# Optimization experiments

Measured on AMD Instinct MI355X. Metric: run time of the kernel, lower is better.

Reference implementation:

```python
import jax, jax.numpy as jnp
import numpy as np

MODES = 128
WIDTH = 128
L_SEG = 20
M_CHEB = 8


def _cft_mag(x):
    # x: [B, C, N] real. Faithful port of vectorized_batched_cft_decomposed
    # (L=20 segments, M=8 Chebyshev nodes), restricted to the first MODES
    # frequencies (the only ones consumed downstream). Returns mean-|CFT|
    # over channels: [B, MODES]. Output is detached in the original code.
    n = x.shape[-1]
    t = jnp.linspace(0.0, 1.0, n)
    freqs = jnp.arange(MODES, dtype=jnp.float32)  # rfftfreq(n, d=1/n)[:MODES]
    seg_len = 1.0 / L_SEG
    a = jnp.linspace(0.0, 1.0, L_SEG + 1)[:-1]  # [L] segment starts
    k = jnp.arange(M_CHEB, dtype=jnp.float32)
    nodes = -jnp.cos((2.0 * k + 1.0) * jnp.pi / (2.0 * M_CHEB))  # [M]
    T = jnp.cos(k[:, None] * jnp.arccos(nodes)[None, :])  # [M(k), M(node)]
    w_prime = freqs * (2.0 * jnp.pi * seg_len / 2.0)  # [F]
    exp_q = jnp.exp(-1j * nodes[:, None] * w_prime[None, :])  # [M, F]
    cheb_w = (T @ exp_q) * (seg_len / 2.0)  # [M, F] complex
    shift = jnp.exp(-1j * 2.0 * jnp.pi * freqs[None, :] * a[:, None])  # [L, F]
    W = shift[:, None, :] * cheb_w[None, :, :]  # [L, M, F]
    # quadrature sample points and linear interpolation from the grid t
    t_seg = a[:, None] + seg_len / 2.0 * (nodes[None, :] + 1.0)  # [L, M]
    right = jnp.minimum(jnp.searchsorted(t, t_seg.reshape(-1)), n - 1).reshape(L_SEG, M_CHEB)
    left = jnp.maximum(right - 1, 0)
    tl, tr = t[left], t[right]
    denom = jnp.where(tr - tl == 0.0, 1.0, tr - tl)
    w_r = (t_seg - tl) / denom
    w_l = 1.0 - w_r
    sig = w_l[None, None] * x[:, :, left] + w_r[None, None] * x[:, :, right]  # [B,C,L,M]
    spec = jnp.einsum('bclm,lmf->bcf', sig.astype(jnp.complex64), W)  # [B,C,F]
    spec = jax.lax.stop_gradient(spec)  # .detach() in the original
    return jnp.mean(jnp.abs(spec), axis=1)  # [B, MODES]


def _forward(x, fc0_W, fc0_b, gate_W, gate_b, wA_re, wA_im, wB_re, wB_im,
             conv_W, conv_b, fc1_W, fc1_b, fc2_W, fc2_b):
    B, N, _ = x.shape
    grid = jnp.broadcast_to(jnp.linspace(0.0, 1.0, N)[None, :, None], (B, N, 1))
    h = jnp.concatenate([x, grid], axis=-1) @ fc0_W.T + fc0_b  # [B,N,W]
    h = h.transpose(0, 2, 1)  # [B,W,N]
    n_f = N // 2 + 1
    for i in range(4):
        mag = _cft_mag(h)  # [B, MODES], detached
        gate = jax.nn.sigmoid(mag @ gate_W[i].T + gate_b[i])  # [B, W]
        # weights1 = gate*A + (1-gate)*B, then the original einsum
        # 'bix,bioy->box' sums weights over the mode axis y; fold that sum
        # into the (in,out) matrices first.
        wA = (wA_re[i] + 1j * wA_im[i]).sum(-1)  # [in, out]
        wB = (wB_re[i] + 1j * wB_im[i]).sum(-1)
        Wg = gate[:, None, :] * wA[None] + (1.0 - gate[:, None, :]) * wB[None]  # [B,in,out]
        h_ft = jnp.fft.rfft(h)  # [B,W,n_f]
        out_modes = jnp.einsum('bif,bio->bof', h_ft[:, :, :MODES], Wg)
        out_ft = jnp.zeros((B, WIDTH, n_f), jnp.complex64).at[:, :, :MODES].set(out_modes)
        x1 = jnp.fft.irfft(out_ft, n=N)  # [B,W,N]
        x2 = jnp.einsum('bcn,oc->bon', h, conv_W[i]) + conv_b[i][None, :, None]
        h = x1 + x2
        if i < 3:
            h = jax.nn.gelu(h, approximate=False)
    h = h.transpose(0, 2, 1)  # [B,N,W]
    h = jax.nn.gelu(h @ fc1_W.T + fc1_b, approximate=False)
    return h @ fc2_W.T + fc2_b  # [B,N,1]


def setup_inputs() -> dict:
    key = jax.random.key(0)
    ks = jax.random.split(key, 16)
    B, N = 64, 4096
    scale = 1.0 / (WIDTH * WIDTH)
    d = {}
    d['x'] = jax.random.normal(ks[0], (B, N, 1), jnp.float32)
    d['fc0_W'] = jax.random.normal(ks[1], (WIDTH, 2), jnp.float32) * 0.1
    d['fc0_b'] = jnp.zeros((WIDTH,), jnp.float32)
    d['gate_W'] = jax.random.normal(ks[2], (4, WIDTH, MODES), jnp.float32) * 0.05
    d['gate_b'] = jnp.zeros((4, WIDTH), jnp.float32)
    d['wA_re'] = jax.random.uniform(ks[3], (4, WIDTH, WIDTH, MODES), jnp.float32) * scale
    d['wA_im'] = jax.random.uniform(ks[4], (4, WIDTH, WIDTH, MODES), jnp.float32) * scale
    d['wB_re'] = jax.random.uniform(ks[5], (4, WIDTH, WIDTH, MODES), jnp.float32) * scale
    d['wB_im'] = jax.random.uniform(ks[6], (4, WIDTH, WIDTH, MODES), jnp.float32) * scale
    d['conv_W'] = jax.random.normal(ks[7], (4, WIDTH, WIDTH), jnp.float32) * 0.05
    d['conv_b'] = jnp.zeros((4, WIDTH), jnp.float32)
    d['fc1_W'] = jax.random.normal(ks[8], (128, WIDTH), jnp.float32) * 0.05
    d['fc1_b'] = jnp.zeros((128,), jnp.float32)
    d['fc2_W'] = jax.random.normal(ks[9], (1, 128), jnp.float32) * 0.05
    d['fc2_b'] = jnp.zeros((1,), jnp.float32)
    return d


def reference(x, fc0_W, fc0_b, gate_W, gate_b, wA_re, wA_im, wB_re, wB_im,
              conv_W, conv_b, fc1_W, fc1_b, fc2_W, fc2_b):
    return _forward(x, fc0_W, fc0_b, gate_W, gate_b, wA_re, wA_im, wB_re, wB_im,
                    conv_W, conv_b, fc1_W, fc1_b, fc2_W, fc2_b)
```

## Files before the change

### kernel.cpp

```cpp
#include <hip/hip_runtime.h>
#include <math.h>

#define B_SZ 64
#define WID 128
#define NPT 4096
#define MODES 128
#define LSEG 20
#define MCH 8
#define LM 160

typedef _Float16 half8 __attribute__((ext_vector_type(8)));
typedef float f32x4 __attribute__((ext_vector_type(4)));

#define LO_SCALE 2048.0f
#define LO_INV   (1.0f/2048.0f)

static constexpr size_t BY_F    = 0;
static constexpr size_t BY_wsum = BY_F + 8388608;
static constexpr size_t BY_Wcre = BY_wsum + 1048576;
static constexpr size_t BY_Wcim = BY_Wcre + 81920;
static constexpr size_t BY_wl   = BY_Wcim + 81920;
static constexpr size_t BY_wr   = BY_wl + 1024;
static constexpr size_t BY_li   = BY_wr + 1024;
static constexpr size_t BY_magp = BY_li + 1024;
static constexpr size_t BY_gate = BY_magp + 524288;
static constexpr size_t BY_hh   = BY_gate + 32768;
static constexpr size_t BY_hl   = BY_hh + 67108864;
static constexpr size_t BY_Tfh  = BY_hl + 67108864;
static constexpr size_t BY_Tfl  = BY_Tfh + 2097152;
static constexpr size_t BY_Tih  = BY_Tfl + 2097152;
static constexpr size_t BY_Til  = BY_Tih + 2097152;
static constexpr size_t BY_Xh   = BY_Til + 2097152;
static constexpr size_t BY_Xl   = BY_Xh + 4194304;
static constexpr size_t BY_cWh  = BY_Xl + 4194304;
static constexpr size_t BY_cWl  = BY_cWh + 131072;
static constexpr size_t BY_f1h  = BY_cWl + 131072;
static constexpr size_t BY_f1l  = BY_f1h + 32768;
static constexpr size_t BY_end  = BY_f1l + 32768;

__device__ __forceinline__ float gelu_f(float x){
    return 0.5f*x*(1.0f+erff(x*0.70710678118654752f));
}
__device__ __forceinline__ void split_f16(float v, _Float16& hi, _Float16& lo){
    hi = (_Float16)v;
    lo = (_Float16)((v - (float)hi)*LO_SCALE);
}

__global__ void k_tables(_Float16* __restrict__ Tfh, _Float16* __restrict__ Tfl,
                         _Float16* __restrict__ Tih, _Float16* __restrict__ Til){
    int idx = blockIdx.x*256 + threadIdx.x;
    int n = idx >> 8, k2 = idx & 255;
    int f = k2 >> 1;
    int m = (n*f) & 4095;
    double th = (double)m * (3.14159265358979323846/2048.0);
    double s, c; sincos(th, &s, &c);
    float vf = (k2&1) ? (float)(-s) : (float)c;
    _Float16 h1,l1; split_f16(vf, h1, l1);
    Tfh[(size_t)k2*4096 + n] = h1;
    Tfl[(size_t)k2*4096 + n] = l1;
    float vi;
    if (k2 == 0)      vi = 1.0f;
    else if (k2 == 1) vi = 0.0f;
    else              vi = vf;
    _Float16 h2,l2; split_f16(vi, h2, l2);
    Tih[(size_t)n*256 + k2] = h2;
    Til[(size_t)n*256 + k2] = l2;
}

__global__ void k_cft_tables(float* __restrict__ Wre, float* __restrict__ Wim,
                             float* __restrict__ wl, float* __restrict__ wr,
                             int* __restrict__ li){
    int idx = blockIdx.x*128 + threadIdx.x;
    if (idx >= LM*MODES) return;
    int lm = idx >> 7;  int f = idx & 127;
    int l = lm / MCH, m = lm % MCH;
    const double PI = 3.14159265358979323846;
    double nodes[8], Tm[8];
    #pragma unroll
    for (int j=0;j<8;j++){
        nodes[j] = -cos((2.0*j+1.0)*PI/16.0);
        Tm[j] = cos((double)m * acos(nodes[j]));
    }
    double wp = (double)f * PI * 0.05;
    double cwre=0.0, cwim=0.0;
    #pragma unroll
    for (int j=0;j<8;j++){
        double sj, cj; sincos(nodes[j]*wp, &sj, &cj);
        cwre += Tm[j]*cj;
        cwim -= Tm[j]*sj;
    }
    cwre *= 0.025; cwim *= 0.025;
    int r = (f*l) % 20;
    double sa = 2.0*PI*(double)r/20.0;
    double shre = cos(sa), shim = -sin(sa);
    Wre[lm*128+f] = (float)(shre*cwre - shim*cwim);
    Wim[lm*128+f] = (float)(shre*cwim + shim*cwre);
    if (f == 0){
        double v = (double)l/20.0 + 0.025*(nodes[m]+1.0);
        int rr = (int)ceil(v*4095.0);
        if (rr > 4095) rr = 4095;
        if (rr < 1) rr = 1;
        int le = rr-1;
        double tl = (double)le/4095.0, tr = (double)rr/4095.0;
        double wrv = (v - tl)/(tr - tl);
        li[lm] = le;
        wl[lm] = (float)(1.0 - wrv);
        wr[lm] = (float)wrv;
    }
}

__global__ void k_wsum(const float* __restrict__ wAre, const float* __restrict__ wAim,
                       const float* __restrict__ wBre, const float* __restrict__ wBim,
                       float* __restrict__ out){
    int row  = blockIdx.x*4 + (threadIdx.x>>6);
    int lane = threadIdx.x & 63;
    const float* src = (blockIdx.y==0)?wAre:(blockIdx.y==1)?wAim:(blockIdx.y==2)?wBre:wBim;
    float v = src[(size_t)row*128 + lane] + src[(size_t)row*128 + 64 + lane];
    #pragma unroll
    for (int o=32;o>0;o>>=1) v += __shfl_down(v, o);
    if (lane==0) out[(size_t)blockIdx.y*65536 + row] = v;
}

__global__ void k_wsplit(const float* __restrict__ convW, const float* __restrict__ fc1W,
                         _Float16* __restrict__ cWh, _Float16* __restrict__ cWl,
                         _Float16* __restrict__ f1h, _Float16* __restrict__ f1l){
    int idx = blockIdx.x*256 + threadIdx.x;
    if (idx < 65536){
        _Float16 hi,lo; split_f16(convW[idx], hi, lo);
        cWh[idx]=hi; cWl[idx]=lo;
    } else {
        int j = idx - 65536;
        _Float16 hi,lo; split_f16(fc1W[j], hi, lo);
        f1h[j]=hi; f1l[j]=lo;
    }
}

__global__ void k_h0(const float* __restrict__ x, const float* __restrict__ w0,
                     const float* __restrict__ b0,
                     _Float16* __restrict__ hh, _Float16* __restrict__ hl){
    int idx = blockIdx.x*256 + threadIdx.x;
    int n8 = idx & 511;
    int w  = (idx >> 9) & 127;
    int b  = idx >> 16;
    int n0 = n8*8;
    float w00 = w0[w*2], w01 = w0[w*2+1], bb = b0[w];
    const float* xr = &x[((size_t)b<<12) + n0];
    float4 x0 = *reinterpret_cast<const float4*>(xr);
    float4 x1 = *reinterpret_cast<const float4*>(xr+4);
    float xv[8]={x0.x,x0.y,x0.z,x0.w,x1.x,x1.y,x1.z,x1.w};
    half8 vh, vl;
    #pragma unroll
    for (int q=0;q<8;q++){
        float g = (float)(n0+q) * (1.0f/4095.0f);
        float v = xv[q]*w00 + g*w01 + bb;
        _Float16 hi,lo; split_f16(v,hi,lo);
        vh[q]=hi; vl[q]=lo;
    }
    size_t o = ((size_t)(b*128+w))*4096 + n0;
    *reinterpret_cast<half8*>(&hh[o]) = vh;
    *reinterpret_cast<half8*>(&hl[o]) = vl;
}

__global__ void k_cft(const _Float16* __restrict__ hh, const _Float16* __restrict__ hl,
                      const float* __restrict__ Wre, const float* __restrict__ Wim,
                      const float* __restrict__ wl, const float* __restrict__ wr,
                      const int* __restrict__ li, float* __restrict__ magp){
    int b = blockIdx.x, cg = blockIdx.y;
    int f = threadIdx.x;
    __shared__ float sig[LM];
    __shared__ float swl[LM], swr[LM];
    __shared__ int   sli[LM];
    for (int s=f; s<LM; s+=128){ swl[s]=wl[s]; swr[s]=wr[s]; sli[s]=li[s]; }
    __syncthreads();
    float acc = 0.f;
    for (int cc=0; cc<8; cc++){
        int c = cg*8 + cc;
        const _Float16* rh = hh + ((size_t)(b*128+c))*4096;
        const _Float16* rl = hl + ((size_t)(b*128+c))*4096;
        for (int s=f; s<LM; s+=128){
            int le = sli[s];
            float v0 = (float)rh[le]   + (float)rl[le]*LO_INV;
            float v1 = (float)rh[le+1] + (float)rl[le+1]*LO_INV;
            sig[s] = swl[s]*v0 + swr[s]*v1;
        }
        __syncthreads();
        float re=0.f, im=0.f;
        #pragma unroll 8
        for (int s=0;s<LM;s++){
            float sv = sig[s];
            re = fmaf(sv, Wre[s*128+f], re);
            im = fmaf(sv, Wim[s*128+f], im);
        }
        acc += sqrtf(re*re+im*im);
        __syncthreads();
    }
    magp[(b*16+cg)*128 + f] = acc;
}

__global__ void k_gate(const float* __restrict__ magp, const float* __restrict__ gW,
                       const float* __restrict__ gB, float* __restrict__ gate, int layer){
    int b = blockIdx.x, w = threadIdx.x;
    __shared__ float ms[128];
    float s = 0.f;
    #pragma unroll
    for (int g=0; g<16; g++) s += magp[(b*16+g)*128 + w];
    ms[w] = s * (1.0f/128.0f);
    __syncthreads();
    const float* gwr = gW + ((size_t)layer*128 + w)*128;
    float a = gB[layer*128 + w];
    #pragma unroll 8
    for (int fq=0; fq<128; fq++) a = fmaf(ms[fq], gwr[fq], a);
    gate[b*128+w] = 1.0f/(1.0f+expf(-a));
}

__global__ __launch_bounds__(256) void k_fdft(
        const _Float16* __restrict__ hh, const _Float16* __restrict__ hl,
        const _Float16* __restrict__ Tfh, const _Float16* __restrict__ Tfl,
        float* __restrict__ F){
    __shared__ _Float16 Ah[2][64][40], Al[2][64][40], Bh[2][64][40], Bl[2][64][40];
    int id = blockIdx.x;
    int swz = (id & 7)*64 + (id >> 3);
    int bx = swz & 3, by = swz >> 2;
    int col0 = bx*64, row0 = by*64;
    int tid = threadIdx.x;
    int lane = tid & 63, w = tid >> 6;
    int wr = (w>>1)*32, wc = (w&1)*32;
    int l15 = lane & 15, l4 = lane >> 4;
    f32x4 acc[2][2] = {}; f32x4 acc2[2][2] = {};
    int srow = tid >> 2, sseg = tid & 3;
    const _Float16* pa_h = hh  + (size_t)(row0+srow)*4096 + sseg*8;
    const _Float16* pa_l = hl  + (size_t)(row0+srow)*4096 + sseg*8;
    const _Float16* pb_h = Tfh + (size_t)(col0+srow)*4096 + sseg*8;
    const _Float16* pb_l = Tfl + (size_t)(col0+srow)*4096 + sseg*8;
    half8 Aah,Aal,Abh,Abl, Bah,Bal,Bbh,Bbl;
#define LOADK(sa,sal,sb,sbl,ck) do{ int kk=(ck)*32; \
    sa  = *reinterpret_cast<const half8*>(pa_h + kk); \
    sal = *reinterpret_cast<const half8*>(pa_l + kk); \
    sb  = *reinterpret_cast<const half8*>(pb_h + kk); \
    sbl = *reinterpret_cast<const half8*>(pb_l + kk); }while(0)
#define WRITEK(sa,sal,sb,sbl,buf) do{ \
    *reinterpret_cast<half8*>(&Ah[buf][srow][sseg*8]) = sa; \
    *reinterpret_cast<half8*>(&Al[buf][srow][sseg*8]) = sal; \
    *reinterpret_cast<half8*>(&Bh[buf][srow][sseg*8]) = sb; \
    *reinterpret_cast<half8*>(&Bl[buf][srow][sseg*8]) = sbl; }while(0)
#define MMF(buf) do{ \
    half8 fah[2], fal[2], fbh[2], fbl[2]; \
    _Pragma("unroll") for (int i=0;i<2;i++){ \
        fah[i] = *reinterpret_cast<const half8*>(&Ah[buf][wr + i*16 + l15][l4*8]); \
        fal[i] = *reinterpret_cast<const half8*>(&Al[buf][wr + i*16 + l15][l4*8]); \
        fbh[i] = *reinterpret_cast<const half8*>(&Bh[buf][wc + i*16 + l15][l4*8]); \
        fbl[i] = *reinterpret_cast<const half8*>(&Bl[buf][wc + i*16 + l15][l4*8]); } \
    _Pragma("unroll") for (int i=0;i<2;i++) \
        _Pragma("unroll") for (int j=0;j<2;j++){ \
            acc[i][j]  = __builtin_amdgcn_mfma_f32_16x16x32_f16(fah[i], fbh[j], acc[i][j], 0,0,0); \
            acc2[i][j] = __builtin_amdgcn_mfma_f32_16x16x32_f16(fah[i], fbl[j], acc2[i][j],0,0,0); \
            acc2[i][j] = __builtin_amdgcn_mfma_f32_16x16x32_f16(fal[i], fbh[j], acc2[i][j],0,0,0); } }while(0)
    LOADK(Aah,Aal,Abh,Abl, 0);
    WRITEK(Aah,Aal,Abh,Abl, 0);
    LOADK(Aah,Aal,Abh,Abl, 1);
    LOADK(Bah,Bal,Bbh,Bbl, 2);
    __syncthreads();
    for (int tt = 0; tt < 64; ++tt){
        int t = tt*2;
        MMF(0);
        WRITEK(Aah,Aal,Abh,Abl, 1);
        if (t+3 < 128) LOADK(Aah,Aal,Abh,Abl, t+3);
        __syncthreads();
        MMF(1);
        if (t+2 < 128) WRITEK(Bah,Bal,Bbh,Bbl, 0);
        if (t+4 < 128) LOADK(Bah,Bal,Bbh,Bbl, t+4);
        __syncthreads();
    }
#undef LOADK
#undef WRITEK
#undef MMF
    #pragma unroll
    for (int i=0;i<2;i++)
        #pragma unroll
        for (int j=0;j<2;j++)
            #pragma unroll
            for (int r=0;r<4;r++){
                int row = row0 + wr + i*16 + l4*4 + r;
                int col = col0 + wc + j*16 + l15;
                F[(size_t)row*256 + col] = acc[i][j][r] + acc2[i][j][r]*LO_INV;
            }
}

__global__ __launch_bounds__(256) void k_modemix(const float* __restrict__ F,
        const float* __restrict__ wsum, const float* __restrict__ gate,
        _Float16* __restrict__ Xh, _Float16* __restrict__ Xl, int layer){
    int b = blockIdx.x, og = blockIdx.y;
    __shared__ float Fs[16][256];
    __shared__ float Wa_re[128][8], Wa_im[128][8], Wb_re[128][8], Wb_im[128][8];
    int tid = threadIdx.x;
    for (int e=tid; e<1024; e+=256){
        int i = e>>3, oo = e&7;
        size_t base = ((size_t)layer*128 + i)*128 + og*8 + oo;
        Wa_re[i][oo] = wsum[0*65536 + base];
        Wa_im[i][oo] = wsum[1*65536 + base];
        Wb_re[i][oo] = wsum[2*65536 + base];
        Wb_im[i][oo] = wsum[3*65536 + base];
    }
    int f = tid & 127, half = tid >> 7;
    float pre[4]={},pim[4]={},qre[4]={},qim[4]={};
    for (int i0=0;i0<128;i0+=16){
        for (int e=tid; e<4096; e+=256){
            int ii = e >> 8, k2 = e & 255;
            Fs[ii][k2] = F[((size_t)(b*128 + i0+ii))*256 + k2];
        }
        __syncthreads();
        #pragma unroll
        for (int ii=0; ii<16; ii++){
            float fre = Fs[ii][2*f], fim = Fs[ii][2*f+1];
            int i = i0+ii;
            #pragma unroll
            for (int q=0;q<4;q++){
                int oo = half*4+q;
                float are=Wa_re[i][oo], aim=Wa_im[i][oo];
                float bre=Wb_re[i][oo], bim=Wb_im[i][oo];
                pre[q] = fmaf(fre, are, fmaf(-fim, aim, pre[q]));
                pim[q] = fmaf(fre, aim, fmaf( fim, are, pim[q]));
                qre[q] = fmaf(fre, bre, fmaf(-fim, bim, qre[q]));
                qim[q] = fmaf(fre, bim, fmaf( fim, bre, qim[q]));
            }
        }
        __syncthreads();
    }
    #pragma unroll
    for (int q=0;q<4;q++){
        int o = og*8 + half*4 + q;
        float g = gate[b*128+o];
        float xre = g*pre[q] + (1.f-g)*qre[q];
        float xim = g*pim[q] + (1.f-g)*qim[q];
        float s = (f==0) ? (1.0f/4096.0f) : (2.0f/4096.0f);
        xre *= s; xim *= s;
        if (f==0) xim = 0.f;
        size_t base = ((size_t)(b*128+o))*256 + 2*f;
        _Float16 h1,l1; split_f16(xre,h1,l1); Xh[base]=h1;   Xl[base]=l1;
        _Float16 h2,l2; split_f16(xim,h2,l2); Xh[base+1]=h2; Xl[base+1]=l2;
    }
}

__global__ __launch_bounds__(256) void k_flayer(
    const _Float16* __restrict__ Xh, const _Float16* __restrict__ Xl,
    const _Float16* __restrict__ Tih, const _Float16* __restrict__ Til,
    const _Float16* __restrict__ cWh, const _Float16* __restrict__ cWl,
    const float* __restrict__ convB,
    _Float16* __restrict__ hh, _Float16* __restrict__ hl,
    int layer, int applyGelu){
    __shared__ _Float16 As_h[2][128][40], As_l[2][128][40];
    __shared__ _Float16 Bs_h[2][64][40],  Bs_l[2][64][40];
    int n0 = blockIdx.x*64;
    int b  = blockIdx.y;
    int tid = threadIdx.x, lane = tid & 63, w = tid >> 6;
    int l15 = lane & 15, l4 = lane >> 4;
    int o0 = w*32;
    int aro = tid >> 2, asl = tid & 3;
    int ctc = tid >> 3, ctn = tid & 7;
    int ocp = ((tid >> 6) ^ (tid & 3));
    const _Float16* cA_h = cWh + (size_t)layer*16384 + (size_t)aro*128 + asl*8;
    const _Float16* cA_l = cWl + (size_t)layer*16384 + (size_t)aro*128 + asl*8;
    const _Float16* xA_h = Xh + ((size_t)(b*128 + aro))*256 + asl*8;
    const _Float16* xA_l = Xl + ((size_t)(b*128 + aro))*256 + asl*8;
    const _Float16* hB_h = hh + ((size_t)(b*128 + ctc))*4096 + n0 + ctn*8;
    const _Float16* hB_l = hl + ((size_t)(b*128 + ctc))*4096 + n0 + ctn*8;
    const _Float16* tB_h = Tih + (size_t)(n0 + aro)*256 + asl*8;
    const _Float16* tB_l = Til + (size_t)(n0 + aro)*256 + asl*8;
    f32x4 acc[2][4] = {}; f32x4 acc2[2][4] = {};
    half8 rA[6], rB[6];
#define LOADR(r,ck) do{ \
    if ((ck) < 4){ int kk = (ck)*32; \
        r[0] = *reinterpret_cast<const half8*>(cA_h + kk); \
        r[1] = *reinterpret_cast<const half8*>(cA_l + kk); \
        r[2] = *reinterpret_cast<const half8*>(cA_h + 64*128 + kk); \
        r[3] = *reinterpret_cast<const half8*>(cA_l + 64*128 + kk); \
        r[4] = *reinterpret_cast<const half8*>(hB_h + (size_t)(ck)*32*4096); \
        r[5] = *reinterpret_cast<const half8*>(hB_l + (size_t)(ck)*32*4096); \
    } else { int kk = ((ck)-4)*32; \
        r[0] = *reinterpret_cast<const half8*>(xA_h + kk); \
        r[1] = *reinterpret_cast<const half8*>(xA_l + kk); \
        r[2] = *reinterpret_cast<const half8*>(xA_h + 64*256 + kk); \
        r[3] = *reinterpret_cast<const half8*>(xA_l + 64*256 + kk); \
        r[4] = *reinterpret_cast<const half8*>(tB_h + kk); \
        r[5] = *reinterpret_cast<const half8*>(tB_l + kk); } }while(0)
#define WRITER(r,buf,ck) do{ \
    *reinterpret_cast<half8*>(&As_h[buf][aro][asl*8])    = r[0]; \
    *reinterpret_cast<half8*>(&As_l[buf][aro][asl*8])    = r[1]; \
    *reinterpret_cast<half8*>(&As_h[buf][aro+64][asl*8]) = r[2]; \
    *reinterpret_cast<half8*>(&As_l[buf][aro+64][asl*8]) = r[3]; \
    if ((ck) < 4){ \
        _Pragma("unroll") for (int j2=0;j2<8;j2++){ \
            int n = ctn*8 + j2; \
            Bs_h[buf][n][ocp*8 + (ctc&7)] = r[4][j2]; \
            Bs_l[buf][n][ocp*8 + (ctc&7)] = r[5][j2]; } \
    } else { \
        *reinterpret_cast<half8*>(&Bs_h[buf][aro][asl*8]) = r[4]; \
        *reinterpret_cast<half8*>(&Bs_l[buf][aro][asl*8]) = r[5]; } }while(0)
#define MML(buf,ck) do{ \
    half8 ah[2], al[2], bh[4], bl[4]; \
    _Pragma("unroll") for (int i=0;i<2;i++){ \
        ah[i] = *reinterpret_cast<const half8*>(&As_h[buf][o0+i*16+l15][l4*8]); \
        al[i] = *reinterpret_cast<const half8*>(&As_l[buf][o0+i*16+l15][l4*8]); } \
    if ((ck) < 4){ \
        _Pragma("unroll") for (int j=0;j<4;j++){ \
            int n = j*16 + l15; int sl = (l4 ^ ((n>>3)&3)); \
            bh[j] = *reinterpret_cast<const half8*>(&Bs_h[buf][n][sl*8]); \
            bl[j] = *reinterpret_cast<const half8*>(&Bs_l[buf][n][sl*8]); } \
    } else { \
        _Pragma("unroll") for (int j=0;j<4;j++){ \
            bh[j] = *reinterpret_cast<const half8*>(&Bs_h[buf][j*16+l15][l4*8]); \
            bl[j] = *reinterpret_cast<const half8*>(&Bs_l[buf][j*16+l15][l4*8]); } } \
    _Pragma("unroll") for (int i=0;i<2;i++) \
        _Pragma("unroll") for (int j=0;j<4;j++){ \
            acc[i][j]  = __builtin_amdgcn_mfma_f32_16x16x32_f16(ah[i], bh[j], acc[i][j], 0,0,0); \
            acc2[i][j] = __builtin_amdgcn_mfma_f32_16x16x32_f16(ah[i], bl[j], acc2[i][j],0,0,0); \
            acc2[i][j] = __builtin_amdgcn_mfma_f32_16x16x32_f16(al[i], bh[j], acc2[i][j],0,0,0); } }while(0)
    LOADR(rA, 0);
    WRITER(rA, 0, 0);
    LOADR(rA, 1);
    LOADR(rB, 2);
    __syncthreads();
    #pragma unroll
    for (int tt=0; tt<6; ++tt){
        const int t = 2*tt;
        MML(0, t);
        WRITER(rA, 1, t+1);
        if (t+3 < 12) LOADR(rA, t+3);
        __syncthreads();
        MML(1, t+1);
        if (t+2 < 12) WRITER(rB, 0, t+2);
        if (t+4 < 12) LOADR(rB, t+4);
        __syncthreads();
    }
#undef LOADR
#undef WRITER
#undef MML
    #pragma unroll
    for (int i=0;i<2;i++)
        #pragma unroll
        for (int j=0;j<4;j++)
            #pragma unroll
            for (int r=0;r<4;r++){
                int o = o0 + i*16 + l4*4 + r;
                int n = n0 + j*16 + l15;
                float v = acc[i][j][r] + acc2[i][j][r]*LO_INV + convB[layer*128+o];
                if (applyGelu) v = gelu_f(v);
                _Float16 hi,lo; split_f16(v,hi,lo);
                size_t oi = ((size_t)(b*128+o))*4096 + n;
                hh[oi] = hi; hl[oi] = lo;
            }
}

__global__ __launch_bounds__(256) void k_head(
        const _Float16* __restrict__ hh, const _Float16* __restrict__ hl,
        const _Float16* __restrict__ f1h, const _Float16* __restrict__ f1l,
        const float* __restrict__ fc1b,
        const float* __restrict__ fc2W, const float* __restrict__ fc2b,
        float* __restrict__ out){
    __shared__ _Float16 Bch[64][136], Bcl[64][136];
    __shared__ _Float16 Ash[128][40], Asl[128][40];
    __shared__ float red[16][64];
    int n0 = blockIdx.x*64;
    int b  = blockIdx.y;
    int tid = threadIdx.x, lane = tid & 63, w = tid >> 6;
    int l15 = lane & 15, l4 = lane >> 4;
    int j0 = w*32;
    {
        int c = tid & 127, nh = tid >> 7;
        const _Float16* rh = hh + ((size_t)(b*128+c))*4096 + n0 + nh*32;
        const _Float16* rl = hl + ((size_t)(b*128+c))*4096 + n0 + nh*32;
        #pragma unroll
        for (int j=0;j<4;j++){
            half8 vhv = *reinterpret_cast<const half8*>(rh + j*8);
            half8 vlv = *reinterpret_cast<const half8*>(rl + j*8);
            #pragma unroll
            for (int q=0;q<8;q++){
                int n = nh*32 + j*8 + q;
                Bch[n][c] = vhv[q];
                Bcl[n][c] = vlv[q];
            }
        }
    }
    __syncthreads();
    int so2 = tid >> 2, sseg = tid & 3;
    f32x4 acc[2][4] = {}; f32x4 acc2[2][4] = {};
    for (int k0=0;k0<128;k0+=32){
        #pragma unroll
        for (int p=0;p<2;p++){
            int o = p*64 + so2;
            *reinterpret_cast<half8*>(&Ash[o][sseg*8]) =
                *reinterpret_cast<const half8*>(&f1h[(size_t)o*128 + k0 + sseg*8]);
            *reinterpret_cast<half8*>(&Asl[o][sseg*8]) =
                *reinterpret_cast<const half8*>(&f1l[(size_t)o*128 + k0 + sseg*8]);
        }
        __syncthreads();
        half8 ah[2],al[2],bh[4],bl[4];
        #pragma unroll
        for (int i=0;i<2;i++){
            ah[i] = *reinterpret_cast<const half8*>(&Ash[j0+i*16+l15][l4*8]);
            al[i] = *reinterpret_cast<const half8*>(&Asl[j0+i*16+l15][l4*8]);
        }
        #pragma unroll
        for (int j=0;j<4;j++){
            bh[j] = *reinterpret_cast<const half8*>(&Bch[j*16+l15][k0+l4*8]);
            bl[j] = *reinterpret_cast<const half8*>(&Bcl[j*16+l15][k0+l4*8]);
        }
        #pragma unroll
        for (int i=0;i<2;i++)
            #pragma unroll
            for (int j=0;j<4;j++){
                acc[i][j]  = __builtin_amdgcn_mfma_f32_16x16x32_f16(ah[i], bh[j], acc[i][j], 0,0,0);
                acc2[i][j] = __builtin_amdgcn_mfma_f32_16x16x32_f16(ah[i], bl[j], acc2[i][j],0,0,0);
                acc2[i][j] = __builtin_amdgcn_mfma_f32_16x16x32_f16(al[i], bh[j], acc2[i][j],0,0,0);
            }
        __syncthreads();
    }
    float part[4];
    #pragma unroll
    for (int j=0;j<4;j++) part[j] = 0.f;
    #pragma unroll
    for (int i=0;i<2;i++){
        #pragma unroll
        for (int r=0;r<4;r++){
            int jj = j0 + i*16 + l4*4 + r;
            float b1 = fc1b[jj];
            float w2 = fc2W[jj];
            #pragma unroll
            for (int j=0;j<4;j++){
                float v = acc[i][j][r] + acc2[i][j][r]*LO_INV + b1;
                part[j] = fmaf(w2, gelu_f(v), part[j]);
            }
        }
    }
    #pragma unroll
    for (int j=0;j<4;j++) red[w*4+l4][j*16+l15] = part[j];
    __syncthreads();
    if (tid < 64){
        float s = fc2b[0];
        #pragma unroll
        for (int r=0;r<16;r++) s += red[r][tid];
        out[((size_t)b<<12) + n0 + tid] = s;
    }
}

extern "C" void kernel_launch(void* const* d_in, const int* in_sizes, int n_in,
                              void* d_out, int out_size, void* d_ws, size_t ws_size,
                              hipStream_t stream) {
    const float* x     = (const float*)d_in[0];
    const float* fc0W  = (const float*)d_in[1];
    const float* fc0b  = (const float*)d_in[2];
    const float* gateW = (const float*)d_in[3];
    const float* gateB = (const float*)d_in[4];
    const float* wAre  = (const float*)d_in[5];
    const float* wAim  = (const float*)d_in[6];
    const float* wBre  = (const float*)d_in[7];
    const float* wBim  = (const float*)d_in[8];
    const float* convW = (const float*)d_in[9];
    const float* convB = (const float*)d_in[10];
    const float* fc1W  = (const float*)d_in[11];
    const float* fc1b  = (const float*)d_in[12];
    const float* fc2W  = (const float*)d_in[13];
    const float* fc2b  = (const float*)d_in[14];
    float* out = (float*)d_out;
    char*  wsb = (char*)d_ws;

    float* F    = (float*)(wsb + BY_F);
    float* wsum = (float*)(wsb + BY_wsum);
    float* Wcre = (float*)(wsb + BY_Wcre);
    float* Wcim = (float*)(wsb + BY_Wcim);
    float* wl   = (float*)(wsb + BY_wl);
    float* wr   = (float*)(wsb + BY_wr);
    int*   li   = (int*)(wsb + BY_li);
    float* magp = (float*)(wsb + BY_magp);
    float* gate = (float*)(wsb + BY_gate);
    _Float16* hh  = (_Float16*)(wsb + BY_hh);
    _Float16* hl  = (_Float16*)(wsb + BY_hl);
    _Float16* Tfh = (_Float16*)(wsb + BY_Tfh);
    _Float16* Tfl = (_Float16*)(wsb + BY_Tfl);
    _Float16* Tih = (_Float16*)(wsb + BY_Tih);
    _Float16* Til = (_Float16*)(wsb + BY_Til);
    _Float16* Xh  = (_Float16*)(wsb + BY_Xh);
    _Float16* Xl  = (_Float16*)(wsb + BY_Xl);
    _Float16* cWh = (_Float16*)(wsb + BY_cWh);
    _Float16* cWl = (_Float16*)(wsb + BY_cWl);
    _Float16* f1h = (_Float16*)(wsb + BY_f1h);
    _Float16* f1l = (_Float16*)(wsb + BY_f1l);

    k_tables<<<4096, 256, 0, stream>>>(Tfh, Tfl, Tih, Til);
    k_cft_tables<<<160, 128, 0, stream>>>(Wcre, Wcim, wl, wr, li);
    k_wsum<<<dim3(16384,4), 256, 0, stream>>>(wAre, wAim, wBre, wBim, wsum);
    k_wsplit<<<320, 256, 0, stream>>>(convW, fc1W, cWh, cWl, f1h, f1l);
    k_h0<<<16384, 256, 0, stream>>>(x, fc0W, fc0b, hh, hl);

    for (int layer=0; layer<4; layer++){
        k_cft<<<dim3(64,16), 128, 0, stream>>>(hh, hl, Wcre, Wcim, wl, wr, li, magp);
        k_gate<<<64, 128, 0, stream>>>(magp, gateW, gateB, gate, layer);
        k_fdft<<<512, 256, 0, stream>>>(hh, hl, Tfh, Tfl, F);
        k_modemix<<<dim3(64,16), 256, 0, stream>>>(F, wsum, gate, Xh, Xl, layer);
        k_flayer<<<dim3(64,64), 256, 0, stream>>>(Xh, Xl, Tih, Til, cWh, cWl, convB,
                                                  hh, hl, layer, layer<3 ? 1:0);
    }
    k_head<<<dim3(64,64), 256, 0, stream>>>(hh, hl, f1h, f1l, fc1b, fc2W, fc2b, out);
    (void)in_sizes; (void)n_in; (void)out_size; (void)ws_size;
}
```

Before: 1.390 ms.

## Pre-swizzle DFT twiddle tables into MFMA fragment layout and load directly to registers

The forward and inverse DFT twiddle tables are now written in the per-lane MFMA B-fragment order, so k_fdft and k_flayer read B operands straight from global memory into registers instead of staging them through LDS. This removes the B-side LDS writes and reads and shrinks shared memory in k_fdft. The cost is more global or L2 traffic per wave, since each wave now fetches its own B fragments with no sharing across the block, and more registers for the prefetched fragments.

```diff
diff --git a/kernel.cpp b/kernel.cpp
--- a/kernel.cpp
+++ b/kernel.cpp
@@ -46,8 +46,8 @@
     lo = (_Float16)((v - (float)hi)*LO_SCALE);
 }
 
-__global__ void k_tables(_Float16* __restrict__ Tfh, _Float16* __restrict__ Tfl,
-                         _Float16* __restrict__ Tih, _Float16* __restrict__ Til){
+__global__ void k_tables(_Float16* __restrict__ Tffh, _Float16* __restrict__ Tffl,
+                         _Float16* __restrict__ Tifh, _Float16* __restrict__ Tifl){
     int idx = blockIdx.x*256 + threadIdx.x;
     int n = idx >> 8, k2 = idx & 255;
     int f = k2 >> 1;
@@ -55,16 +55,26 @@
     double th = (double)m * (3.14159265358979323846/2048.0);
     double s, c; sincos(th, &s, &c);
     float vf = (k2&1) ? (float)(-s) : (float)c;
-    _Float16 h1,l1; split_f16(vf, h1, l1);
-    Tfh[(size_t)k2*4096 + n] = h1;
-    Tfl[(size_t)k2*4096 + n] = l1;
+    {
+        _Float16 h1,l1; split_f16(vf, h1, l1);
+        int ct = k2>>4, ck = n>>5;
+        int lane = (((n>>3)&3)<<4) | (k2&15);
+        int j = n & 7;
+        size_t off = (((size_t)(ct*128 + ck))<<9) + lane*8 + j;
+        Tffh[off] = h1; Tffl[off] = l1;
+    }
     float vi;
     if (k2 == 0)      vi = 1.0f;
     else if (k2 == 1) vi = 0.0f;
     else              vi = vf;
-    _Float16 h2,l2; split_f16(vi, h2, l2);
-    Tih[(size_t)n*256 + k2] = h2;
-    Til[(size_t)n*256 + k2] = l2;
+    {
+        _Float16 h2,l2; split_f16(vi, h2, l2);
+        int nt = n>>4, ck2 = k2>>5;
+        int lane = (((k2>>3)&3)<<4) | (n&15);
+        int j = k2 & 7;
+        size_t off = (((size_t)(nt*8 + ck2))<<9) + lane*8 + j;
+        Tifh[off] = h2; Tifl[off] = l2;
+    }
 }
 
 __global__ void k_cft_tables(float* __restrict__ Wre, float* __restrict__ Wim,
@@ -215,64 +225,65 @@
 
 __global__ __launch_bounds__(256) void k_fdft(
         const _Float16* __restrict__ hh, const _Float16* __restrict__ hl,
-        const _Float16* __restrict__ Tfh, const _Float16* __restrict__ Tfl,
+        const _Float16* __restrict__ Tffh, const _Float16* __restrict__ Tffl,
         float* __restrict__ F){
-    __shared__ _Float16 Ah[2][64][40], Al[2][64][40], Bh[2][64][40], Bl[2][64][40];
+    __shared__ _Float16 Ah[2][64][40], Al[2][64][40];
     int id = blockIdx.x;
     int swz = (id & 7)*64 + (id >> 3);
     int bx = swz & 3, by = swz >> 2;
     int col0 = bx*64, row0 = by*64;
-    int tid = threadIdx.x;
-    int lane = tid & 63, w = tid >> 6;
+    int tid = threadIdx.x, lane = tid & 63, w = tid >> 6;
     int wr = (w>>1)*32, wc = (w&1)*32;
     int l15 = lane & 15, l4 = lane >> 4;
     f32x4 acc[2][2] = {}; f32x4 acc2[2][2] = {};
     int srow = tid >> 2, sseg = tid & 3;
-    const _Float16* pa_h = hh  + (size_t)(row0+srow)*4096 + sseg*8;
-    const _Float16* pa_l = hl  + (size_t)(row0+srow)*4096 + sseg*8;
-    const _Float16* pb_h = Tfh + (size_t)(col0+srow)*4096 + sseg*8;
-    const _Float16* pb_l = Tfl + (size_t)(col0+srow)*4096 + sseg*8;
-    half8 Aah,Aal,Abh,Abl, Bah,Bal,Bbh,Bbl;
-#define LOADK(sa,sal,sb,sbl,ck) do{ int kk=(ck)*32; \
-    sa  = *reinterpret_cast<const half8*>(pa_h + kk); \
-    sal = *reinterpret_cast<const half8*>(pa_l + kk); \
-    sb  = *reinterpret_cast<const half8*>(pb_h + kk); \
-    sbl = *reinterpret_cast<const half8*>(pb_l + kk); }while(0)
-#define WRITEK(sa,sal,sb,sbl,buf) do{ \
-    *reinterpret_cast<half8*>(&Ah[buf][srow][sseg*8]) = sa; \
-    *reinterpret_cast<half8*>(&Al[buf][srow][sseg*8]) = sal; \
-    *reinterpret_cast<half8*>(&Bh[buf][srow][sseg*8]) = sb; \
-    *reinterpret_cast<half8*>(&Bl[buf][srow][sseg*8]) = sbl; }while(0)
-#define MMF(buf) do{ \
-    half8 fah[2], fal[2], fbh[2], fbl[2]; \
+    const _Float16* pa_h = hh + (size_t)(row0+srow)*4096 + sseg*8;
+    const _Float16* pa_l = hl + (size_t)(row0+srow)*4096 + sseg*8;
+    int ct0 = (col0 + wc) >> 4;
+    const _Float16* pfh = Tffh + (size_t)lane*8;
+    const _Float16* pfl = Tffl + (size_t)lane*8;
+    half8 a0h,a0l,a1h,a1l;
+    half8 bf0[4], bf1[4];
+#define LOADA(xh,xl,ck) do{ \
+    xh = *reinterpret_cast<const half8*>(pa_h + (size_t)(ck)*32); \
+    xl = *reinterpret_cast<const half8*>(pa_l + (size_t)(ck)*32); }while(0)
+#define WRITEA(xh,xl,buf) do{ \
+    *reinterpret_cast<half8*>(&Ah[buf][srow][sseg*8]) = xh; \
+    *reinterpret_cast<half8*>(&Al[buf][srow][sseg*8]) = xl; }while(0)
+#define LOADB(dst,ck) do{ \
+    dst[0] = *reinterpret_cast<const half8*>(pfh + (((size_t)(ct0  )*128 + (ck))<<9)); \
+    dst[1] = *reinterpret_cast<const half8*>(pfh + (((size_t)(ct0+1)*128 + (ck))<<9)); \
+    dst[2] = *reinterpret_cast<const half8*>(pfl + (((size_t)(ct0  )*128 + (ck))<<9)); \
+    dst[3] = *reinterpret_cast<const half8*>(pfl + (((size_t)(ct0+1)*128 + (ck))<<9)); }while(0)
+#define MMF(buf,BF) do{ \
     _Pragma("unroll") for (int i=0;i<2;i++){ \
-        fah[i] = *reinterpret_cast<const half8*>(&Ah[buf][wr + i*16 + l15][l4*8]); \
-        fal[i] = *reinterpret_cast<const half8*>(&Al[buf][wr + i*16 + l15][l4*8]); \
-        fbh[i] = *reinterpret_cast<const half8*>(&Bh[buf][wc + i*16 + l15][l4*8]); \
-        fbl[i] = *reinterpret_cast<const half8*>(&Bl[buf][wc + i*16 + l15][l4*8]); } \
-    _Pragma("unroll") for (int i=0;i<2;i++) \
+        half8 fah = *reinterpret_cast<const half8*>(&Ah[buf][wr + i*16 + l15][l4*8]); \
+        half8 fal = *reinterpret_cast<const half8*>(&Al[buf][wr + i*16 + l15][l4*8]); \
         _Pragma("unroll") for (int j=0;j<2;j++){ \
-            acc[i][j]  = __builtin_amdgcn_mfma_f32_16x16x32_f16(fah[i], fbh[j], acc[i][j], 0,0,0); \
-            acc2[i][j] = __builtin_amdgcn_mfma_f32_16x16x32_f16(fah[i], fbl[j], acc2[i][j],0,0,0); \
-            acc2[i][j] = __builtin_amdgcn_mfma_f32_16x16x32_f16(fal[i], fbh[j], acc2[i][j],0,0,0); } }while(0)
-    LOADK(Aah,Aal,Abh,Abl, 0);
-    WRITEK(Aah,Aal,Abh,Abl, 0);
-    LOADK(Aah,Aal,Abh,Abl, 1);
-    LOADK(Bah,Bal,Bbh,Bbl, 2);
+            acc[i][j]  = __builtin_amdgcn_mfma_f32_16x16x32_f16(fah, BF[j],   acc[i][j], 0,0,0); \
+            acc2[i][j] = __builtin_amdgcn_mfma_f32_16x16x32_f16(fah, BF[2+j], acc2[i][j],0,0,0); \
+            acc2[i][j] = __builtin_amdgcn_mfma_f32_16x16x32_f16(fal, BF[j],   acc2[i][j],0,0,0); } } }while(0)
+    LOADA(a0h,a0l,0); WRITEA(a0h,a0l,0);
+    LOADA(a0h,a0l,1);
+    LOADA(a1h,a1l,2);
+    LOADB(bf0,0); LOADB(bf1,1);
     __syncthreads();
-    for (int tt = 0; tt < 64; ++tt){
+    for (int tt=0; tt<64; ++tt){
         int t = tt*2;
-        MMF(0);
-        WRITEK(Aah,Aal,Abh,Abl, 1);
-        if (t+3 < 128) LOADK(Aah,Aal,Abh,Abl, t+3);
-        __syncthreads();
-        MMF(1);
-        if (t+2 < 128) WRITEK(Bah,Bal,Bbh,Bbl, 0);
-        if (t+4 < 128) LOADK(Bah,Bal,Bbh,Bbl, t+4);
-        __syncthreads();
-    }
-#undef LOADK
-#undef WRITEK
+        MMF(0,bf0);
+        WRITEA(a0h,a0l,1);
+        if (t+2 < 128) LOADB(bf0, t+2);
+        if (t+3 < 128) LOADA(a0h,a0l, t+3);
+        __syncthreads();
+        MMF(1,bf1);
+        if (t+2 < 128) WRITEA(a1h,a1l,0);
+        if (t+3 < 128) LOADB(bf1, t+3);
+        if (t+4 < 128) LOADA(a1h,a1l, t+4);
+        __syncthreads();
+    }
+#undef LOADA
+#undef WRITEA
+#undef LOADB
 #undef MMF
     #pragma unroll
     for (int i=0;i<2;i++)
@@ -343,7 +354,7 @@
 
 __global__ __launch_bounds__(256) void k_flayer(
     const _Float16* __restrict__ Xh, const _Float16* __restrict__ Xl,
-    const _Float16* __restrict__ Tih, const _Float16* __restrict__ Til,
+    const _Float16* __restrict__ Tifh, const _Float16* __restrict__ Tifl,
     const _Float16* __restrict__ cWh, const _Float16* __restrict__ cWl,
     const float* __restrict__ convB,
     _Float16* __restrict__ hh, _Float16* __restrict__ hl,
@@ -364,25 +375,25 @@
     const _Float16* xA_l = Xl + ((size_t)(b*128 + aro))*256 + asl*8;
     const _Float16* hB_h = hh + ((size_t)(b*128 + ctc))*4096 + n0 + ctn*8;
     const _Float16* hB_l = hl + ((size_t)(b*128 + ctc))*4096 + n0 + ctn*8;
-    const _Float16* tB_h = Tih + (size_t)(n0 + aro)*256 + asl*8;
-    const _Float16* tB_l = Til + (size_t)(n0 + aro)*256 + asl*8;
+    int nt0 = n0 >> 4;
+    const _Float16* pTh = Tifh + (size_t)lane*8;
+    const _Float16* pTl = Tifl + (size_t)lane*8;
     f32x4 acc[2][4] = {}; f32x4 acc2[2][4] = {};
     half8 rA[6], rB[6];
+    half8 bf0[8], bf1[8];
 #define LOADR(r,ck) do{ \
-    if ((ck) < 4){ int kk = (ck)*32; \
+    if ((ck) < 4){ size_t kk = (size_t)(ck)*32; \
         r[0] = *reinterpret_cast<const half8*>(cA_h + kk); \
         r[1] = *reinterpret_cast<const half8*>(cA_l + kk); \
         r[2] = *reinterpret_cast<const half8*>(cA_h + 64*128 + kk); \
         r[3] = *reinterpret_cast<const half8*>(cA_l + 64*128 + kk); \
         r[4] = *reinterpret_cast<const half8*>(hB_h + (size_t)(ck)*32*4096); \
         r[5] = *reinterpret_cast<const half8*>(hB_l + (size_t)(ck)*32*4096); \
-    } else { int kk = ((ck)-4)*32; \
+    } else { size_t kk = (size_t)((ck)-4)*32; \
         r[0] = *reinterpret_cast<const half8*>(xA_h + kk); \
         r[1] = *reinterpret_cast<const half8*>(xA_l + kk); \
         r[2] = *reinterpret_cast<const half8*>(xA_h + 64*256 + kk); \
-        r[3] = *reinterpret_cast<const half8*>(xA_l + 64*256 + kk); \
-        r[4] = *reinterpret_cast<const half8*>(tB_h + kk); \
-        r[5] = *reinterpret_cast<const half8*>(tB_l + kk); } }while(0)
+        r[3] = *reinterpret_cast<const half8*>(xA_l + 64*256 + kk); } }while(0)
 #define WRITER(r,buf,ck) do{ \
     *reinterpret_cast<half8*>(&As_h[buf][aro][asl*8])    = r[0]; \
     *reinterpret_cast<half8*>(&As_l[buf][aro][asl*8])    = r[1]; \
@@ -390,31 +401,29 @@
     *reinterpret_cast<half8*>(&As_l[buf][aro+64][asl*8]) = r[3]; \
     if ((ck) < 4){ \
         _Pragma("unroll") for (int j2=0;j2<8;j2++){ \
-            int n = ctn*8 + j2; \
-            Bs_h[buf][n][ocp*8 + (ctc&7)] = r[4][j2]; \
-            Bs_l[buf][n][ocp*8 + (ctc&7)] = r[5][j2]; } \
-    } else { \
-        *reinterpret_cast<half8*>(&Bs_h[buf][aro][asl*8]) = r[4]; \
-        *reinterpret_cast<half8*>(&Bs_l[buf][aro][asl*8]) = r[5]; } }while(0)
-#define MML(buf,ck) do{ \
-    half8 ah[2], al[2], bh[4], bl[4]; \
-    _Pragma("unroll") for (int i=0;i<2;i++){ \
-        ah[i] = *reinterpret_cast<const half8*>(&As_h[buf][o0+i*16+l15][l4*8]); \
-        al[i] = *reinterpret_cast<const half8*>(&As_l[buf][o0+i*16+l15][l4*8]); } \
+            int n1 = ctn*8 + j2; \
+            Bs_h[buf][n1][ocp*8 + (ctc&7)] = r[4][j2]; \
+            Bs_l[buf][n1][ocp*8 + (ctc&7)] = r[5][j2]; } } }while(0)
+#define LOADBF(dst,ckp) do{ \
+    _Pragma("unroll") for (int j=0;j<4;j++){ \
+        dst[j]   = *reinterpret_cast<const half8*>(pTh + (((size_t)((nt0+j)*8 + (ckp)))<<9)); \
+        dst[4+j] = *reinterpret_cast<const half8*>(pTl + (((size_t)((nt0+j)*8 + (ckp)))<<9)); } }while(0)
+#define MML(buf,ck,BF) do{ \
+    half8 bh[4], bl[4]; \
     if ((ck) < 4){ \
         _Pragma("unroll") for (int j=0;j<4;j++){ \
             int n = j*16 + l15; int sl = (l4 ^ ((n>>3)&3)); \
             bh[j] = *reinterpret_cast<const half8*>(&Bs_h[buf][n][sl*8]); \
             bl[j] = *reinterpret_cast<const half8*>(&Bs_l[buf][n][sl*8]); } \
     } else { \
+        _Pragma("unroll") for (int j=0;j<4;j++){ bh[j] = BF[j]; bl[j] = BF[4+j]; } } \
+    _Pragma("unroll") for (int i=0;i<2;i++){ \
+        half8 ah = *reinterpret_cast<const half8*>(&As_h[buf][o0+i*16+l15][l4*8]); \
+        half8 al = *reinterpret_cast<const half8*>(&As_l[buf][o0+i*16+l15][l4*8]); \
         _Pragma("unroll") for (int j=0;j<4;j++){ \
-            bh[j] = *reinterpret_cast<const half8*>(&Bs_h[buf][j*16+l15][l4*8]); \
-            bl[j] = *reinterpret_cast<const half8*>(&Bs_l[buf][j*16+l15][l4*8]); } } \
-    _Pragma("unroll") for (int i=0;i<2;i++) \
-        _Pragma("unroll") for (int j=0;j<4;j++){ \
-            acc[i][j]  = __builtin_amdgcn_mfma_f32_16x16x32_f16(ah[i], bh[j], acc[i][j], 0,0,0); \
-            acc2[i][j] = __builtin_amdgcn_mfma_f32_16x16x32_f16(ah[i], bl[j], acc2[i][j],0,0,0); \
-            acc2[i][j] = __builtin_amdgcn_mfma_f32_16x16x32_f16(al[i], bh[j], acc2[i][j],0,0,0); } }while(0)
+            acc[i][j]  = __builtin_amdgcn_mfma_f32_16x16x32_f16(ah, bh[j], acc[i][j], 0,0,0); \
+            acc2[i][j] = __builtin_amdgcn_mfma_f32_16x16x32_f16(ah, bl[j], acc2[i][j],0,0,0); \
+            acc2[i][j] = __builtin_amdgcn_mfma_f32_16x16x32_f16(al, bh[j], acc2[i][j],0,0,0); } } }while(0)
     LOADR(rA, 0);
     WRITER(rA, 0, 0);
     LOADR(rA, 1);
@@ -423,17 +432,20 @@
     #pragma unroll
     for (int tt=0; tt<6; ++tt){
         const int t = 2*tt;
-        MML(0, t);
+        MML(0, t, bf0);
         WRITER(rA, 1, t+1);
+        if (t+2 >= 4 && t+2 < 12) LOADBF(bf0, t+2-4);
         if (t+3 < 12) LOADR(rA, t+3);
         __syncthreads();
-        MML(1, t+1);
+        MML(1, t+1, bf1);
         if (t+2 < 12) WRITER(rB, 0, t+2);
+        if (t+3 >= 4 && t+3 < 12) LOADBF(bf1, t+3-4);
         if (t+4 < 12) LOADR(rB, t+4);
         __syncthreads();
     }
 #undef LOADR
 #undef WRITER
+#undef LOADBF
 #undef MML
     #pragma unroll
     for (int i=0;i<2;i++)
@@ -573,20 +585,20 @@
     int*   li   = (int*)(wsb + BY_li);
     float* magp = (float*)(wsb + BY_magp);
     float* gate = (float*)(wsb + BY_gate);
-    _Float16* hh  = (_Float16*)(wsb + BY_hh);
-    _Float16* hl  = (_Float16*)(wsb + BY_hl);
-    _Float16* Tfh = (_Float16*)(wsb + BY_Tfh);
-    _Float16* Tfl = (_Float16*)(wsb + BY_Tfl);
-    _Float16* Tih = (_Float16*)(wsb + BY_Tih);
-    _Float16* Til = (_Float16*)(wsb + BY_Til);
-    _Float16* Xh  = (_Float16*)(wsb + BY_Xh);
-    _Float16* Xl  = (_Float16*)(wsb + BY_Xl);
-    _Float16* cWh = (_Float16*)(wsb + BY_cWh);
-    _Float16* cWl = (_Float16*)(wsb + BY_cWl);
-    _Float16* f1h = (_Float16*)(wsb + BY_f1h);
-    _Float16* f1l = (_Float16*)(wsb + BY_f1l);
-
-    k_tables<<<4096, 256, 0, stream>>>(Tfh, Tfl, Tih, Til);
+    _Float16* hh   = (_Float16*)(wsb + BY_hh);
+    _Float16* hl   = (_Float16*)(wsb + BY_hl);
+    _Float16* Tffh = (_Float16*)(wsb + BY_Tfh);
+    _Float16* Tffl = (_Float16*)(wsb + BY_Tfl);
+    _Float16* Tifh = (_Float16*)(wsb + BY_Tih);
+    _Float16* Tifl = (_Float16*)(wsb + BY_Til);
+    _Float16* Xh   = (_Float16*)(wsb + BY_Xh);
+    _Float16* Xl   = (_Float16*)(wsb + BY_Xl);
+    _Float16* cWh  = (_Float16*)(wsb + BY_cWh);
+    _Float16* cWl  = (_Float16*)(wsb + BY_cWl);
+    _Float16* f1h  = (_Float16*)(wsb + BY_f1h);
+    _Float16* f1l  = (_Float16*)(wsb + BY_f1l);
+
+    k_tables<<<4096, 256, 0, stream>>>(Tffh, Tffl, Tifh, Tifl);
     k_cft_tables<<<160, 128, 0, stream>>>(Wcre, Wcim, wl, wr, li);
     k_wsum<<<dim3(16384,4), 256, 0, stream>>>(wAre, wAim, wBre, wBim, wsum);
     k_wsplit<<<320, 256, 0, stream>>>(convW, fc1W, cWh, cWl, f1h, f1l);
@@ -595,9 +607,9 @@
     for (int layer=0; layer<4; layer++){
         k_cft<<<dim3(64,16), 128, 0, stream>>>(hh, hl, Wcre, Wcim, wl, wr, li, magp);
         k_gate<<<64, 128, 0, stream>>>(magp, gateW, gateB, gate, layer);
-        k_fdft<<<512, 256, 0, stream>>>(hh, hl, Tfh, Tfl, F);
+        k_fdft<<<512, 256, 0, stream>>>(hh, hl, Tffh, Tffl, F);
         k_modemix<<<dim3(64,16), 256, 0, stream>>>(F, wsum, gate, Xh, Xl, layer);
-        k_flayer<<<dim3(64,64), 256, 0, stream>>>(Xh, Xl, Tih, Til, cWh, cWl, convB,
+        k_flayer<<<dim3(64,64), 256, 0, stream>>>(Xh, Xl, Tifh, Tifl, cWh, cWl, convB,
                                                   hh, hl, layer, layer<3 ? 1:0);
     }
     k_head<<<dim3(64,64), 256, 0, stream>>>(hh, hl, f1h, f1l, fc1b, fc2W, fc2b, out);
```

After: 1.356 ms. 1.03x faster.
